# Performance work log

Measured on AMD Instinct MI355X. Metric: run time of the kernel, lower is better.

## Reference

```python
import jax, jax.numpy as jnp
import numpy as np

N, F, F_, H = 8192, 512, 64, 8
NEG = -1e10

def setup_inputs() -> dict:
    key = jax.random.key(0)
    k1, k2, k3, k4 = jax.random.split(key, 4)
    X = jax.random.normal(k1, (N, F), dtype=jnp.float32)
    A = jax.random.randint(k2, (N, N), 0, 2).astype(jnp.float32)  # dense 0/1 adjacency
    kernels = jax.random.normal(k3, (H, F, F_), dtype=jnp.float32) * 0.05
    attn_kernels = jax.random.normal(k4, (H, 2 * F_), dtype=jnp.float32) * 0.05
    return {"X": X, "A": A, "kernels": kernels, "attn_kernels": attn_kernels}

def reference(X, A, kernels, attn_kernels):
    # Per-head linear transform: [H, N, F_]
    WX = jnp.einsum('nf,hfo->hno', X, kernels)
    a1 = attn_kernels[:, :F_]   # [H, F_] acts on source (row) node
    a2 = attn_kernels[:, F_:]   # [H, F_] acts on target (col) node
    # score[h,i,j] = a1_h . WX[h,i] + a2_h . WX[h,j]  (outer sum, no N^2*2F_ tensor)
    s1 = jnp.einsum('hno,ho->hn', WX, a1)  # [H, N]
    s2 = jnp.einsum('hno,ho->hn', WX, a2)  # [H, N]
    scores = s1[:, :, None] + s2[:, None, :]  # [H, N, N]
    # adjacency mask: A==0 -> -1e10 (note: original has no LeakyReLU)
    masked = jnp.where(A[None, :, :] == 0.0, scores + NEG, scores)
    attn = jax.nn.softmax(masked, axis=-1)  # [H, N, N]
    # dropout is identity at inference (Keras Dropout without training=True)
    feats = jnp.einsum('hnm,hmo->hno', attn, WX)  # [H, N, F_]
    feats = jax.nn.relu(feats)  # concat reduction applies activation per head
    out = jnp.transpose(feats, (1, 0, 2)).reshape(N, H * F_)  # concat heads
    return out
```

## Files before the change

### kernel.cpp

```cpp
#include <hip/hip_runtime.h>
#include <cstdint>

#define NN 8192
#define FF 512
#define FO 64
#define NH 8
#define LDYE 520
#define YPART (8192 * 520)
#define SPLITK 3


typedef __attribute__((ext_vector_type(8))) __bf16 bf16x8;
typedef __attribute__((ext_vector_type(4))) float f32x4;

__device__ __forceinline__ unsigned short f2bf(float f) {
    unsigned int u = __float_as_uint(f);
    u += 0x7fffu + ((u >> 16) & 1u);
    return (unsigned short)(u >> 16);
}

__device__ __forceinline__ void gload16(const void* g, void* l) {
    __builtin_amdgcn_global_load_lds(
        (const __attribute__((address_space(1))) unsigned int*)g,
        (__attribute__((address_space(3))) unsigned int*)l,
        16, 0, 0);
}

__global__ __launch_bounds__(256) void k_convA8(const float* __restrict__ A,
                                                unsigned char* __restrict__ Ab) {
    const size_t gid = (size_t)blockIdx.x * 256 + threadIdx.x;
    const int row127 = (int)(gid & 127);
    const int k16 = (int)((gid >> 7) & 511);
    const int rt = (int)(gid >> 16);
    const uint4* src = (const uint4*)(A + (((size_t)(rt * 128 + row127)) << 13) + k16 * 16);
    uint4 f0 = src[0], f1 = src[1], f2 = src[2], f3 = src[3];
#define PK8(v) (((v.x >> 22) & 0x38u) | (((v.y >> 22) & 0x38u) << 8) | \
                (((v.z >> 22) & 0x38u) << 16) | (((v.w >> 22) & 0x38u) << 24))
    uint4 o = {PK8(f0), PK8(f1), PK8(f2), PK8(f3)};
#undef PK8
    *(uint4*)(Ab + (gid << 4)) = o;
}

__global__ __launch_bounds__(256) void k_prep(const float* __restrict__ X,
                                              const float* __restrict__ Kw,
                                              unsigned short* __restrict__ Xb,
                                              unsigned short* __restrict__ Ktb) {
    const int b = blockIdx.x;
    const int t = threadIdx.x;
    if (b < 2048) {
        size_t base = ((size_t)b * 256 + t) * 8;
        float4 a = *(const float4*)(X + base);
        float4 c = *(const float4*)(X + base + 4);
        ushort4 o0, o1;
        o0.x = f2bf(a.x); o0.y = f2bf(a.y); o0.z = f2bf(a.z); o0.w = f2bf(a.w);
        o1.x = f2bf(c.x); o1.y = f2bf(c.y); o1.z = f2bf(c.z); o1.w = f2bf(c.w);
        *(ushort4*)(Xb + base) = o0;
        *(ushort4*)(Xb + base + 4) = o1;
    } else {
        int h = b - 2048;
        for (int e = t; e < FF * FO; e += 256) {
            int o = e >> 9, f = e & 511;
            Ktb[(size_t)h * FF * FO + e] = f2bf(Kw[(size_t)h * FF * FO + (size_t)f * FO + o]);
        }
    }
}

union WxSmem {
    struct { unsigned short Xs[4096]; unsigned short Ks[2048]; } s;
    unsigned char Vs[64][144];
};

__global__ __launch_bounds__(256) void k_wx(const unsigned short* __restrict__ Xb,
                                            const unsigned short* __restrict__ Ktb,
                                            const float* __restrict__ Aw,
                                            unsigned char* __restrict__ Vt) {
    __shared__ WxSmem sm;
    const int t = threadIdx.x;
    const int n0 = blockIdx.x * 128;
    const int h = blockIdx.y;
    const int lane = t & 63, w = t >> 6;
    const int quad = lane >> 4, l15 = lane & 15;

    const unsigned short* xS0 = Xb + (size_t)(n0 + (t & 127)) * FF + (t >> 7) * 8;
    const unsigned short* xS1 = Xb + (size_t)(n0 + ((t + 256) & 127)) * FF + ((t + 256) >> 7) * 8;
    unsigned short* xD0 = sm.s.Xs + t * 8;
    unsigned short* xD1 = sm.s.Xs + (t + 256) * 8;
    const unsigned short* kS = Ktb + (size_t)h * FF * FO + (size_t)(t & 63) * FF + (t >> 6) * 8;
    unsigned short* kD = sm.s.Ks + t * 8;

    const bf16x8* aF[2];
    const bf16x8* bF[4];
    for (int i = 0; i < 2; ++i)
        aF[i] = (const bf16x8*)(sm.s.Xs + (size_t)(quad * 128 + w * 32 + i * 16 + l15) * 8);
    for (int j = 0; j < 4; ++j)
        bF[j] = (const bf16x8*)(sm.s.Ks + (size_t)(quad * 64 + j * 16 + l15) * 8);

    f32x4 acc[2][4] = {};
    for (int f0 = 0; f0 < FF; f0 += 32) {
        gload16(xS0 + f0, xD0);
        gload16(xS1 + f0, xD1);
        gload16(kS + f0, kD);
        __syncthreads();
        bf16x8 av[2], bv[4];
        for (int i = 0; i < 2; ++i) av[i] = aF[i][0];
        for (int j = 0; j < 4; ++j) bv[j] = bF[j][0];
        for (int i = 0; i < 2; ++i)
            for (int j = 0; j < 4; ++j)
                acc[i][j] = __builtin_amdgcn_mfma_f32_16x16x32_bf16(av[i], bv[j], acc[i][j], 0, 0, 0);
        __syncthreads();
    }

    float a2v[4];
    for (int j = 0; j < 4; ++j) a2v[j] = Aw[h * 128 + 64 + j * 16 + l15];
    float ex[2][4];
    for (int i = 0; i < 2; ++i)
        for (int r = 0; r < 4; ++r) {
            float p = acc[i][0][r] * a2v[0] + acc[i][1][r] * a2v[1]
                    + acc[i][2][r] * a2v[2] + acc[i][3][r] * a2v[3];
            p += __shfl_xor(p, 1);
            p += __shfl_xor(p, 2);
            p += __shfl_xor(p, 4);
            p += __shfl_xor(p, 8);
            ex[i][r] = __expf(p);
        }

    for (int i = 0; i < 2; ++i)
        for (int j = 0; j < 4; ++j) {
            int rowb = w * 32 + i * 16 + quad * 4;
            int col = j * 16 + l15;
            unsigned u = __builtin_amdgcn_cvt_pk_fp8_f32(
                ex[i][0] * acc[i][j][0], ex[i][1] * acc[i][j][1], 0, false);
            u = __builtin_amdgcn_cvt_pk_fp8_f32(
                ex[i][2] * acc[i][j][2], ex[i][3] * acc[i][j][3], (int)u, true);
            *(unsigned*)&sm.Vs[col][rowb] = u;
        }
    __syncthreads();
    for (int j2 = 0; j2 < 2; ++j2) {
        int vid = t + j2 * 256;
        int o = vid >> 3, k16o = vid & 7;
        size_t H = (size_t)((n0 >> 4) + k16o) * 640 + h * 64 + o;
        *(uint4*)(Vt + (H << 4)) = *(const uint4*)&sm.Vs[o][k16o * 16];
    }
    if (l15 == 0) {
        for (int i = 0; i < 2; ++i)
            for (int r = 0; r < 4; ++r) {
                int row = w * 32 + i * 16 + quad * 4 + r;
                unsigned u = __builtin_amdgcn_cvt_pk_fp8_f32(ex[i][r], ex[i][r], 0, false);
                size_t H = (size_t)((n0 >> 4) + (row >> 4)) * 640 + 512 + h;
                Vt[(H << 4) + (row & 15)] = (unsigned char)(u & 0xff);
            }
    }
}

__global__ __launch_bounds__(256) void k_gemm(const unsigned char* __restrict__ Ab,
                                              const unsigned char* __restrict__ Vt,
                                              float* __restrict__ Y) {
    __shared__ unsigned char As0[8192], As1[8192];
    __shared__ unsigned char Bs0[10240], Bs1[10240];
    const int t = threadIdx.x;
    const int id = blockIdx.x;
    const int xcd = id & 7;
    const int u = id >> 3;
    const int ct = u & 3;
    const int rp = ((u >> 2) << 3) | xcd;
    const int rt = rp & 63;
    const int part = rp >> 6;
    const int ks0 = (part * 128) / SPLITK;
    const int ks1 = ((part + 1) * 128) / SPLITK;

    const unsigned char* aS0 = Ab + ((size_t)rt << 20) + (size_t)t * 16;
    const unsigned char* aS1 = aS0 + 4096;
    const int g1 = t + 256, g2 = t + 512;
    const unsigned char* bS0 = Vt + (size_t)((t / 160) * 10240 + (ct * 160 + t % 160) * 16);
    const unsigned char* bS1 = Vt + (size_t)((g1 / 160) * 10240 + (ct * 160 + g1 % 160) * 16);
    const unsigned char* bS2 = Vt + (size_t)((g2 / 160) * 10240 + (ct * 160 + g2 % 160) * 16);

    const int lane = t & 63;
    const int w = t >> 6;
    const int wm = w >> 1, wn = w & 1;
    const int quad = lane >> 4, l15 = lane & 15;

    int aOff[4], bOff[5];
    for (int i = 0; i < 4; ++i)
        aOff[i] = (quad >> 1) * 2048 + (quad & 1) * 8 + (wm * 64 + i * 16 + l15) * 16;
    for (int j = 0; j < 5; ++j)
        bOff[j] = (quad >> 1) * 2560 + (quad & 1) * 8 + (wn * 80 + j * 16 + l15) * 16;

    f32x4 acc[4][5] = {};

#define STAGE(ks, AD, BD)                                                      \
    do {                                                                       \
        const size_t koA = (size_t)(ks) << 13;                                 \
        const size_t koB = (size_t)(ks) * 40960;                               \
        gload16(aS0 + koA, (AD) + t * 16);                                     \
        gload16(aS1 + koA, (AD) + 4096 + t * 16);                              \
        gload16(bS0 + koB, (BD) + t * 16);                                     \
        gload16(bS1 + koB, (BD) + g1 * 16);                                    \
        if (t < 128) gload16(bS2 + koB, (BD) + g2 * 16);                       \
    } while (0)

#define MFMA_TILE(AS, BS)                                                      \
    do {                                                                       \
        _Pragma("unroll")                                                      \
        for (int h2 = 0; h2 < 2; ++h2) {                                       \
            long long av[4], bv[5];                                            \
            for (int i = 0; i < 4; ++i)                                        \
                av[i] = *(const long long*)((AS) + aOff[i] + h2 * 4096);       \
            for (int j = 0; j < 5; ++j)                                        \
                bv[j] = *(const long long*)((BS) + bOff[j] + h2 * 5120);       \
            for (int i = 0; i < 4; ++i)                                        \
                for (int j = 0; j < 5; ++j)                                    \
                    acc[i][j] = __builtin_amdgcn_mfma_f32_16x16x32_fp8_fp8(    \
                        av[i], bv[j], acc[i][j], 0, 0, 0);                     \
        }                                                                      \
    } while (0)

    STAGE(ks0, As0, Bs0);
    __syncthreads();
    int p = 0;
    for (int ks = ks0; ks < ks1; ++ks) {
        if (p == 0) {
            if (ks + 1 < ks1) STAGE(ks + 1, As1, Bs1);
            MFMA_TILE(As0, Bs0);
        } else {
            if (ks + 1 < ks1) STAGE(ks + 1, As0, Bs0);
            MFMA_TILE(As1, Bs1);
        }
        __syncthreads();
        p ^= 1;
    }
#undef STAGE
#undef MFMA_TILE

    float* Yp = Y + (size_t)part * YPART;
    for (int i = 0; i < 4; ++i) {
        int row = rt * 128 + wm * 64 + i * 16 + quad * 4;
        for (int j = 0; j < 5; ++j) {
            int col = ct * 160 + wn * 80 + j * 16 + l15;
            if (col < 520) {
                for (int r = 0; r < 4; ++r)
                    Yp[(size_t)(row + r) * LDYE + col] = acc[i][j][r];
            }
        }
    }
}

__global__ __launch_bounds__(256) void k_epi(const float* __restrict__ Y,
                                             float* __restrict__ out) {
    int idx = blockIdx.x * 256 + threadIdx.x;
    int n = idx >> 7;
    int c = (idx & 127) * 4;
    int h = c >> 6;
    float4 u = {0.f, 0.f, 0.f, 0.f};
    float den = 0.f;
    const float* yp = Y + (size_t)n * LDYE;
#pragma unroll
    for (int p = 0; p < SPLITK; ++p) {
        float4 v = *(const float4*)(yp + c);
        u.x += v.x; u.y += v.y; u.z += v.z; u.w += v.w;
        den += yp[512 + h];
        yp += (size_t)YPART;
    }
    float inv = 1.0f / den;
    float4 o;
    o.x = fmaxf(u.x * inv, 0.f);
    o.y = fmaxf(u.y * inv, 0.f);
    o.z = fmaxf(u.z * inv, 0.f);
    o.w = fmaxf(u.w * inv, 0.f);
    *(float4*)(out + (size_t)n * 512 + c) = o;
}

extern "C" void kernel_launch(void* const* d_in, const int* in_sizes, int n_in,
                              void* d_out, int out_size, void* d_ws, size_t ws_size,
                              hipStream_t stream) {
    const float* X  = (const float*)d_in[0];
    const float* A  = (const float*)d_in[1];
    const float* Kw = (const float*)d_in[2];
    const float* Aw = (const float*)d_in[3];
    float* out = (float*)d_out;
    char* ws = (char*)d_ws;
    unsigned char* Ab = (unsigned char*)ws;
    unsigned char* Vt = (unsigned char*)(ws + (size_t)67108864);
    float* Yb = (float*)(ws + (size_t)67108864 + (size_t)5242880);
    unsigned short* Xb = (unsigned short*)Yb;
    unsigned short* Ktb = Xb + (size_t)NN * FF;

    k_convA8<<<dim3(16384), dim3(256), 0, stream>>>(A, Ab);
    k_prep<<<dim3(2056), dim3(256), 0, stream>>>(X, Kw, Xb, Ktb);
    k_wx<<<dim3(64, 8), dim3(256), 0, stream>>>(Xb, Ktb, Aw, Vt);
    k_gemm<<<dim3(768), dim3(256), 0, stream>>>(Ab, Vt, Yb);
    k_epi<<<dim3(4096), dim3(256), 0, stream>>>(Yb, out);
}
```

Before: 561.7 us.

## Warp-specialize fp8 attention GEMM into producer and MFMA waves, retile to 7 column tiles

Splits the 256-thread block into two MFMA waves and two loader waves: one wave stages A tiles and one stages B tiles into double-buffered LDS. Column tiles shrink from 160 to 80 (7 tiles covering 520 columns), and split-K drops from 3 to 2, giving 896 blocks. The aim is to overlap global-to-LDS loads with MFMA work and cut the partial-sum traffic the epilogue reads. The trade-off is that half the waves do no math, so MFMA throughput per block halves, and the per-block B tile is smaller, so A is reloaded more often per column.

```diff
diff --git a/kernel.cpp b/kernel.cpp
--- a/kernel.cpp
+++ b/kernel.cpp
@@ -7,7 +7,7 @@
 #define NH 8
 #define LDYE 520
 #define YPART (8192 * 520)
-#define SPLITK 3
+#define SPLITK 2
 
 
 typedef __attribute__((ext_vector_type(8))) __bf16 bf16x8;
@@ -156,47 +156,52 @@
                                               const unsigned char* __restrict__ Vt,
                                               float* __restrict__ Y) {
     __shared__ unsigned char As0[8192], As1[8192];
-    __shared__ unsigned char Bs0[10240], Bs1[10240];
+    __shared__ unsigned char Bs0[5120], Bs1[5120];
     const int t = threadIdx.x;
     const int id = blockIdx.x;
     const int xcd = id & 7;
     const int u = id >> 3;
-    const int ct = u & 3;
-    const int rp = ((u >> 2) << 3) | xcd;
+    const int ct = u % 7;
+    const int gq = u / 7;
+    const int rp = gq * 8 + xcd;
     const int rt = rp & 63;
     const int part = rp >> 6;
-    const int ks0 = (part * 128) / SPLITK;
-    const int ks1 = ((part + 1) * 128) / SPLITK;
-
-    const unsigned char* aS0 = Ab + ((size_t)rt << 20) + (size_t)t * 16;
-    const unsigned char* aS1 = aS0 + 4096;
-    const int g1 = t + 256, g2 = t + 512;
-    const unsigned char* bS0 = Vt + (size_t)((t / 160) * 10240 + (ct * 160 + t % 160) * 16);
-    const unsigned char* bS1 = Vt + (size_t)((g1 / 160) * 10240 + (ct * 160 + g1 % 160) * 16);
-    const unsigned char* bS2 = Vt + (size_t)((g2 / 160) * 10240 + (ct * 160 + g2 % 160) * 16);
+    const int ks0 = part * 64;
+    const int ks1 = ks0 + 64;
 
     const int lane = t & 63;
     const int w = t >> 6;
-    const int wm = w >> 1, wn = w & 1;
     const int quad = lane >> 4, l15 = lane & 15;
+
+    const unsigned char* aBase = Ab + ((size_t)rt << 20);
+    int bsrc[5];
+    for (int r = 0; r < 5; ++r) {
+        int g = r * 64 + lane;
+        bsrc[r] = (g / 80) * 10240 + (ct * 80 + g % 80) * 16;
+    }
 
     int aOff[4], bOff[5];
     for (int i = 0; i < 4; ++i)
-        aOff[i] = (quad >> 1) * 2048 + (quad & 1) * 8 + (wm * 64 + i * 16 + l15) * 16;
+        aOff[i] = (quad >> 1) * 2048 + (quad & 1) * 8 + (w * 64 + i * 16 + l15) * 16;
     for (int j = 0; j < 5; ++j)
-        bOff[j] = (quad >> 1) * 2560 + (quad & 1) * 8 + (wn * 80 + j * 16 + l15) * 16;
+        bOff[j] = (quad >> 1) * 1280 + (quad & 1) * 8 + (j * 16 + l15) * 16;
 
     f32x4 acc[4][5] = {};
 
-#define STAGE(ks, AD, BD)                                                      \
+#define STAGE_A(ks, AD)                                                        \
     do {                                                                       \
-        const size_t koA = (size_t)(ks) << 13;                                 \
-        const size_t koB = (size_t)(ks) * 40960;                               \
-        gload16(aS0 + koA, (AD) + t * 16);                                     \
-        gload16(aS1 + koA, (AD) + 4096 + t * 16);                              \
-        gload16(bS0 + koB, (BD) + t * 16);                                     \
-        gload16(bS1 + koB, (BD) + g1 * 16);                                    \
-        if (t < 128) gload16(bS2 + koB, (BD) + g2 * 16);                       \
+        const unsigned char* s = aBase + ((size_t)(ks) << 13) + lane * 16;     \
+        _Pragma("unroll")                                                      \
+        for (int r = 0; r < 8; ++r)                                            \
+            gload16(s + r * 1024, (AD) + (r * 64 + lane) * 16);                \
+    } while (0)
+
+#define STAGE_B(ks, BD)                                                        \
+    do {                                                                       \
+        const unsigned char* s = Vt + (size_t)(ks) * 40960;                    \
+        _Pragma("unroll")                                                      \
+        for (int r = 0; r < 5; ++r)                                            \
+            gload16(s + bsrc[r], (BD) + (r * 64 + lane) * 16);                 \
     } while (0)
 
 #define MFMA_TILE(AS, BS)                                                      \
@@ -207,7 +212,7 @@
             for (int i = 0; i < 4; ++i)                                        \
                 av[i] = *(const long long*)((AS) + aOff[i] + h2 * 4096);       \
             for (int j = 0; j < 5; ++j)                                        \
-                bv[j] = *(const long long*)((BS) + bOff[j] + h2 * 5120);       \
+                bv[j] = *(const long long*)((BS) + bOff[j] + h2 * 2560);       \
             for (int i = 0; i < 4; ++i)                                        \
                 for (int j = 0; j < 5; ++j)                                    \
                     acc[i][j] = __builtin_amdgcn_mfma_f32_16x16x32_fp8_fp8(    \
@@ -215,31 +220,41 @@
         }                                                                      \
     } while (0)
 
-    STAGE(ks0, As0, Bs0);
+    if (w == 2) STAGE_A(ks0, As0);
+    else if (w == 3) STAGE_B(ks0, Bs0);
     __syncthreads();
     int p = 0;
     for (int ks = ks0; ks < ks1; ++ks) {
         if (p == 0) {
-            if (ks + 1 < ks1) STAGE(ks + 1, As1, Bs1);
-            MFMA_TILE(As0, Bs0);
+            if (w < 2) MFMA_TILE(As0, Bs0);
+            else if (ks + 1 < ks1) {
+                if (w == 2) STAGE_A(ks + 1, As1);
+                else STAGE_B(ks + 1, Bs1);
+            }
         } else {
-            if (ks + 1 < ks1) STAGE(ks + 1, As0, Bs0);
-            MFMA_TILE(As1, Bs1);
+            if (w < 2) MFMA_TILE(As1, Bs1);
+            else if (ks + 1 < ks1) {
+                if (w == 2) STAGE_A(ks + 1, As0);
+                else STAGE_B(ks + 1, Bs0);
+            }
         }
         __syncthreads();
         p ^= 1;
     }
-#undef STAGE
+#undef STAGE_A
+#undef STAGE_B
 #undef MFMA_TILE
 
-    float* Yp = Y + (size_t)part * YPART;
-    for (int i = 0; i < 4; ++i) {
-        int row = rt * 128 + wm * 64 + i * 16 + quad * 4;
-        for (int j = 0; j < 5; ++j) {
-            int col = ct * 160 + wn * 80 + j * 16 + l15;
-            if (col < 520) {
-                for (int r = 0; r < 4; ++r)
-                    Yp[(size_t)(row + r) * LDYE + col] = acc[i][j][r];
+    if (w < 2) {
+        float* Yp = Y + (size_t)part * YPART;
+        for (int i = 0; i < 4; ++i) {
+            int row = rt * 128 + w * 64 + i * 16 + quad * 4;
+            for (int j = 0; j < 5; ++j) {
+                int col = ct * 80 + j * 16 + l15;
+                if (col < 520) {
+                    for (int r = 0; r < 4; ++r)
+                        Yp[(size_t)(row + r) * LDYE + col] = acc[i][j][r];
+                }
             }
         }
     }
@@ -288,6 +303,6 @@
     k_convA8<<<dim3(16384), dim3(256), 0, stream>>>(A, Ab);
     k_prep<<<dim3(2056), dim3(256), 0, stream>>>(X, Kw, Xb, Ktb);
     k_wx<<<dim3(64, 8), dim3(256), 0, stream>>>(Xb, Ktb, Aw, Vt);
-    k_gemm<<<dim3(768), dim3(256), 0, stream>>>(Ab, Vt, Yb);
+    k_gemm<<<dim3(896), dim3(256), 0, stream>>>(Ab, Vt, Yb);
     k_epi<<<dim3(4096), dim3(256), 0, stream>>>(Yb, out);
 }
```

New measurement: 563.6 us. Within noise of the previous version (+0.3%).
